# Optimization experiments

Measured on AMD Instinct MI355X. Metric: run time of the kernel, lower is better.

## Reference

```python
import jax, jax.numpy as jnp
import numpy as np

N_SRC, N_TGT, E, L, C_OUT = 100000, 200000, 500000, 256, 2


def setup_inputs() -> dict:
    key = jax.random.key(0)
    ks = jax.random.split(key, 10)
    s = 1.0 / np.sqrt(L)
    return {
        "pos_source": jax.random.normal(ks[0], (N_SRC, 3), jnp.float32),
        "pos_target": jax.random.normal(ks[1], (N_TGT, 3), jnp.float32),
        "latents": jax.random.normal(ks[2], (N_SRC, L), jnp.float32),
        "row": jax.random.randint(ks[3], (E,), 0, N_TGT),
        "col": jax.random.randint(ks[4], (E,), 0, N_SRC),
        "W_in": jax.random.normal(ks[5], (L + 3, L), jnp.float32) * s,
        "b_in": jnp.zeros((L,), jnp.float32),
        "W1": jax.random.normal(ks[6], (L, L), jnp.float32) * s,
        "b1": jnp.zeros((L,), jnp.float32),
        "W2": jax.random.normal(ks[7], (L, L), jnp.float32) * s,
        "b2": jnp.zeros((L,), jnp.float32),
        "W_out": jax.random.normal(ks[8], (L, C_OUT), jnp.float32) * s,
        "b_out": jnp.zeros((C_OUT,), jnp.float32),
    }


def reference(pos_source, pos_target, latents, row, col,
              W_in, b_in, W1, b1, W2, b2, W_out, b_out):
    # gather relative positions and latents per neighbor pair: [E, 3], [E, L]
    pos_rel = pos_target[row] - pos_source[col]
    x = jnp.concatenate([latents[col], pos_rel], axis=1)  # [E, L+3]
    x = x @ W_in + b_in                                   # fc_in
    x = jax.nn.relu(x) @ W1 + b1                          # mlp layer 0 (act first)
    x = jax.nn.relu(x) @ W2 + b2                          # mlp layer 1
    x = x @ W_out + b_out                                 # fc_out (no activation)
    return x[:, 0]                                        # predictions
```

## Files before the change

### kernel.cpp

```cpp
#include <hip/hip_runtime.h>
#include <hip/hip_bf16.h>
#include <stdint.h>

typedef __attribute__((ext_vector_type(8))) short bf16x8;
typedef __attribute__((ext_vector_type(4))) float f32x4;

#define NSRC 100000
#define WIN_OFF 0
#define W1P_OFF (128*1024)
#define BU_OFF  (256*1024)
#define SS_OFF  (BU_OFF + 2048)
#define Y_OFF   (264*1024)

#define PAIRB 1040
#define XBYTES (32*PAIRB)
#define POFF(r) (((r)>>1)*PAIRB + ((r)&1)*512)

#define L32 1040

#define AS3U32(p) ((__attribute__((address_space(3))) uint32_t*)(uintptr_t)(p))
#define AS1U32(p) ((const __attribute__((address_space(1))) uint32_t*)(uintptr_t)(p))

__global__ __launch_bounds__(256) void pack_kernel(
    const float* __restrict__ Win, const float* __restrict__ W1,
    const float* __restrict__ W2, const float* __restrict__ Wout,
    const float* __restrict__ b1, const float* __restrict__ b2,
    const float* __restrict__ b_out, char* __restrict__ wp)
{
    const int t = threadIdx.x, blk = blockIdx.x;
    if (blk < 16) {
        const float* W = (blk < 8) ? Win : W1;
        char* dst = wp + ((blk < 8) ? WIN_OFF : W1P_OFF);
        const int c = blk & 7;
        #pragma unroll
        for (int q = 0; q < 4; ++q) {
            union { bf16x8 v; __hip_bfloat16 h[8]; } u;
            #pragma unroll
            for (int j = 0; j < 8; ++j)
                u.h[j] = __float2bfloat16(W[(size_t)(c*32 + q*8 + j)*256 + t]);
            *(bf16x8*)(dst + c*16384 + t*64 + q*16) = u.v;
        }
    } else if (blk < 24) {
        __shared__ float w0s[256];
        w0s[t] = Wout[t*2];
        __syncthreads();
        const int b = blk - 16, fl = t >> 3, sub = t & 7, f = b*32 + fl;
        const float* row = W2 + (size_t)f*256 + sub*32;
        float p = 0.f;
        #pragma unroll
        for (int j = 0; j < 32; ++j) p += row[j]*w0s[sub*32 + j];
        p += __shfl_xor(p,1); p += __shfl_xor(p,2); p += __shfl_xor(p,4);
        if (sub == 0) {
            float2 v; v.x = b1[f]; v.y = p;
            *(float2*)(wp + BU_OFF + f*8) = v;
        }
    } else {
        __shared__ float rb[4];
        float v = b2[t]*Wout[t*2];
        v += __shfl_xor(v,1); v += __shfl_xor(v,2); v += __shfl_xor(v,4);
        v += __shfl_xor(v,8); v += __shfl_xor(v,16); v += __shfl_xor(v,32);
        if ((t&63) == 0) rb[t>>6] = v;
        __syncthreads();
        if (t == 0) *(float*)(wp + SS_OFF) = rb[0]+rb[1]+rb[2]+rb[3] + b_out[0];
    }
}

__global__ __launch_bounds__(256, 2) void precompute_y(
    const float* __restrict__ latents, const float* __restrict__ b_in,
    const char* __restrict__ wp, char* __restrict__ Yc)
{
    __shared__ __align__(16) char Ls[2][32*L32];
    __shared__ float binS[256];
    const int tid = threadIdx.x, wave = tid >> 6, lane = tid & 63;
    const int q = lane >> 4, lm = lane & 15;

    bf16x8 wA[4][8];
    {
        const char* wb = wp + WIN_OFF;
        #pragma unroll
        for (int mt = 0; mt < 4; ++mt) {
            const int m = wave*64 + mt*16 + lm;
            #pragma unroll
            for (int c = 0; c < 8; ++c)
                wA[mt][c] = *(const bf16x8*)(wb + c*16384 + m*64 + q*16);
        }
    }
    binS[tid] = b_in[tid];

    const int nt32 = NSRC / 32;
    const int t0 = blockIdx.x;

    #define STAGE32(t, buf) do {                                               \
        const float* __lat = latents + (size_t)(t)*32*256;                     \
        _Pragma("unroll")                                                      \
        for (int j = 0; j < 8; ++j) {                                          \
            const int r = wave*8 + j;                                          \
            __builtin_amdgcn_global_load_lds(                                  \
                AS1U32((const char*)(__lat + (size_t)r*256) + lane*16),        \
                AS3U32((buf) + r*L32), 16, 0, 0);                              \
        }                                                                      \
    } while (0)

    if (t0 < nt32) STAGE32(t0, Ls[0]);

    int it = 0;
    for (int t = t0; t < nt32; t += 512, ++it) {
        const int p = it & 1;
        __syncthreads();
        if (t + 512 < nt32) STAGE32(t + 512, Ls[1 - p]);

        f32x4 acc[4][2];
        #pragma unroll
        for (int mt = 0; mt < 4; ++mt)
            #pragma unroll
            for (int nt = 0; nt < 2; ++nt) acc[mt][nt] = (f32x4){0.f,0.f,0.f,0.f};

        const char* lb = Ls[p];
        #pragma unroll
        for (int c = 0; c < 8; ++c) {
            bf16x8 b[2];
            #pragma unroll
            for (int nt = 0; nt < 2; ++nt) {
                const int n = nt*16 + lm;
                const float* fp = (const float*)(lb + n*L32 + c*128 + q*32);
                float4 f0 = *(const float4*)fp;
                float4 f1 = *(const float4*)(fp + 4);
                union { bf16x8 v; __hip_bfloat16 h[8]; } u;
                u.h[0]=__float2bfloat16(f0.x); u.h[1]=__float2bfloat16(f0.y);
                u.h[2]=__float2bfloat16(f0.z); u.h[3]=__float2bfloat16(f0.w);
                u.h[4]=__float2bfloat16(f1.x); u.h[5]=__float2bfloat16(f1.y);
                u.h[6]=__float2bfloat16(f1.z); u.h[7]=__float2bfloat16(f1.w);
                b[nt] = u.v;
            }
            #pragma unroll
            for (int mt = 0; mt < 4; ++mt)
                #pragma unroll
                for (int nt = 0; nt < 2; ++nt)
                    acc[mt][nt] = __builtin_amdgcn_mfma_f32_16x16x32_bf16(wA[mt][c], b[nt], acc[mt][nt], 0,0,0);
        }
        #pragma unroll
        for (int mt = 0; mt < 4; ++mt) {
            const int f0 = wave*64 + mt*16 + q*4;
            float4 bb = *(const float4*)&binS[f0];
            float bbv[4] = {bb.x, bb.y, bb.z, bb.w};
            #pragma unroll
            for (int nt = 0; nt < 2; ++nt) {
                const int srow = t*32 + nt*16 + lm;
                union { uint2 uu; __hip_bfloat16 hh[4]; } pk;
                #pragma unroll
                for (int rg = 0; rg < 4; ++rg)
                    pk.hh[rg] = __float2bfloat16(acc[mt][nt][rg] + bbv[rg]);
                *(uint2*)(Yc + (size_t)srow*512 + f0*2) = pk.uu;
            }
        }
    }
    #undef STAGE32
}

__global__ __launch_bounds__(256, 2) void interp_main(
    const float* __restrict__ pos_src, const float* __restrict__ pos_tgt,
    const int* __restrict__ rowi, const int* __restrict__ coli,
    const float* __restrict__ Win, const char* __restrict__ wp,
    const char* __restrict__ Yc, float* __restrict__ out,
    int E, int ntiles)
{
    __shared__ __align__(16) char Xs[2][XBYTES];
    __shared__ float wposI[32][24];
    __shared__ float buS[512];
    __shared__ float posrel[2][64][4];
    __shared__ int   colsS[2][64];
    __shared__ float red[4][64];

    const int tid = threadIdx.x, wave = tid >> 6, lane = tid & 63;
    const int q = lane >> 4, lm = lane & 15;
    const int bid = blockIdx.x;

    bf16x8 wA[4][8];
    {
        const char* wb = wp + W1P_OFF;
        #pragma unroll
        for (int mt = 0; mt < 4; ++mt) {
            const int m = wave*64 + mt*16 + lm;
            #pragma unroll
            for (int c = 0; c < 8; ++c)
                wA[mt][c] = *(const bf16x8*)(wb + c*16384 + m*64 + q*16);
        }
    }
    {
        #pragma unroll
        for (int s = 0; s < 3; ++s)
            wposI[tid >> 3][s*8 + (tid & 7)] = Win[(size_t)(256+s)*256 + tid];
        *(float2*)&buS[tid*2] = *(const float2*)(wp + BU_OFF + tid*8);
    }
    const float Sv = *(const float*)(wp + SS_OFF);
    const int niter = (ntiles - bid + 511) / 512;

    #pragma unroll
    for (int ii = 0; ii < 2; ++ii) {
        if (tid < 64) {
            long tt = (long)bid + (long)ii*512; if (tt >= ntiles) tt = ntiles - 1;
            long e = tt*64 + tid; if (e >= E) e = E - 1;
            int ri = rowi[e], ci = coli[e];
            colsS[ii][tid] = ci;
            float4 pr;
            pr.x = pos_tgt[ri*3+0] - pos_src[ci*3+0];
            pr.y = pos_tgt[ri*3+1] - pos_src[ci*3+1];
            pr.z = pos_tgt[ri*3+2] - pos_src[ci*3+2];
            pr.w = 0.f;
            *(float4*)&posrel[ii][tid][0] = pr;
        }
    }
    __syncthreads();
    {
        #pragma unroll
        for (int k2 = 0; k2 < 8; ++k2) {
            const int r0 = wave*16 + k2*2;
            const int row = r0 + (lane >> 5);
            const int cv = colsS[0][row];
            const char* src = Yc + (size_t)cv*512 + (lane & 31)*16;
            __builtin_amdgcn_global_load_lds(AS1U32(src), AS3U32(Xs[0] + (r0>>1)*PAIRB), 16, 0, 0);
        }
    }

    for (int i = 0; i < niter; ++i) {
        const int p = i & 1;
        __syncthreads();

        if (i > 0 && tid < 64) {
            long e = ((long)bid + (long)(i-1)*512)*64 + tid;
            if (e < E) out[e] = red[0][tid]+red[1][tid]+red[2][tid]+red[3][tid] + Sv;
        }
        int m_ci = 0; float4 m_pr = {0.f,0.f,0.f,0.f};
        if (tid < 64) {
            long tt = (long)bid + (long)(i+2)*512; if (tt >= ntiles) tt = ntiles - 1;
            long e = tt*64 + tid; if (e >= E) e = E - 1;
            int ri = rowi[e]; m_ci = coli[e];
            m_pr.x = pos_tgt[ri*3+0] - pos_src[m_ci*3+0];
            m_pr.y = pos_tgt[ri*3+1] - pos_src[m_ci*3+1];
            m_pr.z = pos_tgt[ri*3+2] - pos_src[m_ci*3+2];
        }
        {
            const int fs = tid & 31, rb = tid >> 5;
            float w0v[8], w1v[8], w2v[8];
            {
                const float* wi = &wposI[fs][0];
                #pragma unroll
                for (int j = 0; j < 8; ++j) { w0v[j]=wi[j]; w1v[j]=wi[8+j]; w2v[j]=wi[16+j]; }
            }
            char* xb = Xs[p];
            #pragma unroll
            for (int ii2 = 0; ii2 < 8; ++ii2) {
                const int r = rb*8 + ii2;
                float4 pr = *(const float4*)&posrel[p][r][0];
                char* addr = xb + POFF(r) + fs*16;
                union { bf16x8 v; __hip_bfloat16 h[8]; } u;
                u.v = *(bf16x8*)addr;
                #pragma unroll
                for (int j = 0; j < 8; ++j) {
                    float vv = __bfloat162float(u.h[j]) + pr.x*w0v[j] + pr.y*w1v[j] + pr.z*w2v[j];
                    u.h[j] = __float2bfloat16(vv < 0.f ? 0.f : vv);
                }
                *(bf16x8*)addr = u.v;
            }
        }
        __syncthreads();

        {
            const int s = 1 - p;
            char* xb = Xs[s];
            #pragma unroll
            for (int k2 = 0; k2 < 8; ++k2) {
                const int r0 = wave*16 + k2*2;
                const int row = r0 + (lane >> 5);
                const int cv = colsS[s][row];
                const char* src = Yc + (size_t)cv*512 + (lane & 31)*16;
                __builtin_amdgcn_global_load_lds(AS1U32(src), AS3U32(xb + (r0>>1)*PAIRB), 16, 0, 0);
            }
        }
        f32x4 acc[4][4];
        #pragma unroll
        for (int mt = 0; mt < 4; ++mt)
            #pragma unroll
            for (int nt = 0; nt < 4; ++nt) acc[mt][nt] = (f32x4){0.f,0.f,0.f,0.f};
        {
            const char* xb = Xs[p];
            #pragma unroll
            for (int c = 0; c < 8; ++c) {
                bf16x8 b[4];
                #pragma unroll
                for (int nt = 0; nt < 4; ++nt)
                    b[nt] = *(const bf16x8*)(xb + POFF(nt*16+lm) + c*64 + q*16);
                #pragma unroll
                for (int mt = 0; mt < 4; ++mt)
                    #pragma unroll
                    for (int nt = 0; nt < 4; ++nt)
                        acc[mt][nt] = __builtin_amdgcn_mfma_f32_16x16x32_bf16(wA[mt][c], b[nt], acc[mt][nt], 0,0,0);
            }
        }
        float partial[4] = {0.f,0.f,0.f,0.f};
        #pragma unroll
        for (int mt = 0; mt < 4; ++mt) {
            const int f0 = wave*64 + mt*16 + q*4;
            float4 bu0 = *(const float4*)&buS[f0*2];
            float4 bu1 = *(const float4*)&buS[f0*2 + 4];
            float b1v[4] = {bu0.x, bu0.z, bu1.x, bu1.z};
            float uv[4]  = {bu0.y, bu0.w, bu1.y, bu1.w};
            #pragma unroll
            for (int nt = 0; nt < 4; ++nt)
                #pragma unroll
                for (int rg = 0; rg < 4; ++rg) {
                    float h = acc[mt][nt][rg] + b1v[rg];
                    if (h > 0.f) partial[nt] += h * uv[rg];
                }
        }
        #pragma unroll
        for (int nt = 0; nt < 4; ++nt) {
            float v = partial[nt];
            v += __shfl_xor(v, 16);
            v += __shfl_xor(v, 32);
            if (lane < 16) red[wave][nt*16 + lane] = v;
        }
        if (tid < 64) {
            colsS[p][tid] = m_ci;
            *(float4*)&posrel[p][tid][0] = m_pr;
        }
    }
    __syncthreads();
    if (tid < 64) {
        long e = ((long)bid + (long)(niter-1)*512)*64 + tid;
        if (e < E) out[e] = red[0][tid]+red[1][tid]+red[2][tid]+red[3][tid] + Sv;
    }
}

extern "C" void kernel_launch(void* const* d_in, const int* in_sizes, int n_in,
                              void* d_out, int out_size, void* d_ws, size_t ws_size,
                              hipStream_t stream)
{
    const float* pos_src = (const float*)d_in[0];
    const float* pos_tgt = (const float*)d_in[1];
    const float* latents = (const float*)d_in[2];
    const int*   rowi    = (const int*)d_in[3];
    const int*   coli    = (const int*)d_in[4];
    const float* Win     = (const float*)d_in[5];
    const float* b_in    = (const float*)d_in[6];
    const float* W1      = (const float*)d_in[7];
    const float* b1      = (const float*)d_in[8];
    const float* W2      = (const float*)d_in[9];
    const float* b2      = (const float*)d_in[10];
    const float* Wout    = (const float*)d_in[11];
    const float* b_out   = (const float*)d_in[12];
    float* out = (float*)d_out;
    const int E = in_sizes[3];
    const int ntiles = (E + 63) / 64;

    char* wp = (char*)d_ws;
    char* Yc = wp + Y_OFF;

    pack_kernel<<<25, 256, 0, stream>>>(Win, W1, W2, Wout, b1, b2, b_out, wp);
    precompute_y<<<512, 256, 0, stream>>>(latents, b_in, wp, Yc);
    interp_main<<<512, 256, 0, stream>>>(pos_src, pos_tgt, rowi, coli,
                                         Win, wp, Yc, out, E, ntiles);
}
```

Measured before the change: 304.5 us.

## Bucket edges by source-column group and stage group latents into LDS

Adds a slot kernel that bins edges into groups of 64 source columns using atomic counters, with a fixed per-group capacity. A new interp_col kernel stages each group's precomputed Y rows into LDS with one contiguous load, then processes that group's edges in tiles of 64. This replaces random per-edge 512-byte gathers of Y with coalesced loads. The cost is an extra atomic binning pass and padding waste in partially filled tiles. Any edges beyond the per-group capacity of 512 would be silently dropped.

Measured after the change: 448.0 us. +47.1%, slower.

```diff
diff --git a/kernel.cpp b/kernel.cpp
--- a/kernel.cpp
+++ b/kernel.cpp
@@ -12,6 +12,11 @@
 #define SS_OFF  (BU_OFF + 2048)
 #define Y_OFF   (264*1024)
 
+#define NG   1563
+#define CAP  512
+#define CNT_OFF  (Y_OFF + (size_t)NSRC*512 + 32768)
+#define SLOT_OFF (CNT_OFF + 8192)
+
 #define PAIRB 1040
 #define XBYTES (32*PAIRB)
 #define POFF(r) (((r)>>1)*PAIRB + ((r)&1)*512)
@@ -25,7 +30,8 @@
     const float* __restrict__ Win, const float* __restrict__ W1,
     const float* __restrict__ W2, const float* __restrict__ Wout,
     const float* __restrict__ b1, const float* __restrict__ b2,
-    const float* __restrict__ b_out, char* __restrict__ wp)
+    const float* __restrict__ b_out, char* __restrict__ wp,
+    int* __restrict__ cntA)
 {
     const int t = threadIdx.x, blk = blockIdx.x;
     if (blk < 16) {
@@ -54,7 +60,7 @@
             float2 v; v.x = b1[f]; v.y = p;
             *(float2*)(wp + BU_OFF + f*8) = v;
         }
-    } else {
+    } else if (blk == 24) {
         __shared__ float rb[4];
         float v = b2[t]*Wout[t*2];
         v += __shfl_xor(v,1); v += __shfl_xor(v,2); v += __shfl_xor(v,4);
@@ -62,6 +68,22 @@
         if ((t&63) == 0) rb[t>>6] = v;
         __syncthreads();
         if (t == 0) *(float*)(wp + SS_OFF) = rb[0]+rb[1]+rb[2]+rb[3] + b_out[0];
+    } else {
+        const int idx = (blk - 25)*256 + t;
+        if (idx < NG) cntA[idx] = 0;
+    }
+}
+
+__global__ __launch_bounds__(256) void slot_kernel(
+    const int* __restrict__ coli, int* __restrict__ cntA,
+    int* __restrict__ slots, int E)
+{
+    int i = blockIdx.x*256 + threadIdx.x;
+    for (; i < E; i += gridDim.x*256) {
+        const int c = coli[i];
+        const int g = c >> 6;
+        const int p = atomicAdd(&cntA[g], 1);
+        if (p < CAP) slots[(size_t)g*CAP + p] = (i << 6) | (c & 63);
     }
 }
 
@@ -155,6 +177,182 @@
         }
     }
     #undef STAGE32
+}
+
+__global__ __launch_bounds__(256, 2) void interp_col(
+    const float* __restrict__ pos_src, const float* __restrict__ pos_tgt,
+    const int* __restrict__ rowi, const float* __restrict__ Win,
+    const char* __restrict__ wp, const char* __restrict__ Yc,
+    const int* __restrict__ cntA, const int* __restrict__ slots,
+    float* __restrict__ out)
+{
+    __shared__ __align__(16) char Xs[XBYTES];
+    __shared__ __align__(16) char yS[64*512];
+    __shared__ float wposI[32][24];
+    __shared__ float buS[512];
+    __shared__ float posrel[64][4];
+    __shared__ int   lcS[64];
+    __shared__ float red[4][64];
+
+    const int tid = threadIdx.x, wave = tid >> 6, lane = tid & 63;
+    const int q = lane >> 4, lm = lane & 15;
+    const int bid = blockIdx.x;
+
+    bf16x8 wA[4][8];
+    {
+        const char* wb = wp + W1P_OFF;
+        #pragma unroll
+        for (int mt = 0; mt < 4; ++mt) {
+            const int m = wave*64 + mt*16 + lm;
+            #pragma unroll
+            for (int c = 0; c < 8; ++c)
+                wA[mt][c] = *(const bf16x8*)(wb + c*16384 + m*64 + q*16);
+        }
+    }
+    {
+        #pragma unroll
+        for (int s = 0; s < 3; ++s)
+            wposI[tid >> 3][s*8 + (tid & 7)] = Win[(size_t)(256+s)*256 + tid];
+        *(float2*)&buS[tid*2] = *(const float2*)(wp + BU_OFF + tid*8);
+    }
+    const float Sv = *(const float*)(wp + SS_OFF);
+
+    #define STAGE_Y(g) do {                                                    \
+        const char* __src = Yc + (size_t)(g)*32768;                            \
+        _Pragma("unroll")                                                      \
+        for (int j = 0; j < 8; ++j) {                                          \
+            const int base = j*4096 + wave*1024;                               \
+            __builtin_amdgcn_global_load_lds(                                  \
+                AS1U32(__src + base + lane*16), AS3U32(yS + base), 16, 0, 0);  \
+        }                                                                      \
+    } while (0)
+
+    #define CLAMPC(x) ((x) < 0 ? 0 : ((x) > CAP ? CAP : (x)))
+
+    #define META_LOAD(gm, tm, cm) do {                                         \
+        m_eid = -1; m_lc = 0;                                                  \
+        m_pr.x = 0.f; m_pr.y = 0.f; m_pr.z = 0.f; m_pr.w = 0.f;                \
+        if (tid < 64 && (gm) < NG) {                                           \
+            const int j = (tm)*64 + tid;                                       \
+            if (j < (cm)) {                                                    \
+                const int sv = slots[(size_t)(gm)*CAP + j];                    \
+                const int eid = sv >> 6;                                       \
+                m_lc = sv & 63;                                                \
+                const int ri = rowi[eid];                                      \
+                const int cc = (gm)*64 + m_lc;                                 \
+                m_pr.x = pos_tgt[ri*3+0] - pos_src[cc*3+0];                    \
+                m_pr.y = pos_tgt[ri*3+1] - pos_src[cc*3+1];                    \
+                m_pr.z = pos_tgt[ri*3+2] - pos_src[cc*3+2];                    \
+                m_eid = eid;                                                   \
+            }                                                                  \
+        }                                                                      \
+    } while (0)
+
+    int m_eid, m_lc; float4 m_pr;
+    int eidP = -1;
+
+    {
+        const int cg = CLAMPC(cntA[bid]);
+        STAGE_Y(bid);
+        META_LOAD(bid, 0, cg);
+    }
+
+    for (int g = bid; g < NG; g += 512) {
+        const int cnt0 = CLAMPC(cntA[g]);
+        int ntg = (cnt0 + 63) >> 6; if (ntg < 1) ntg = 1;
+        for (int t = 0; t < ntg; ++t) {
+            __syncthreads();
+            if (tid < 64) {
+                if (eidP >= 0)
+                    out[eidP] = red[0][tid]+red[1][tid]+red[2][tid]+red[3][tid] + Sv;
+                *(float4*)&posrel[tid][0] = m_pr;
+                lcS[tid] = m_lc;
+                eidP = m_eid;
+            }
+            __syncthreads();
+            {
+                const int fs = tid & 31, rb = tid >> 5;
+                float w0v[8], w1v[8], w2v[8];
+                {
+                    const float* wi = &wposI[fs][0];
+                    #pragma unroll
+                    for (int j = 0; j < 8; ++j) { w0v[j]=wi[j]; w1v[j]=wi[8+j]; w2v[j]=wi[16+j]; }
+                }
+                #pragma unroll
+                for (int ii2 = 0; ii2 < 8; ++ii2) {
+                    const int r = rb*8 + ii2;
+                    float4 pr = *(const float4*)&posrel[r][0];
+                    const int lc = lcS[r];
+                    union { bf16x8 v; __hip_bfloat16 h[8]; } u;
+                    u.v = *(const bf16x8*)(yS + lc*512 + fs*16);
+                    #pragma unroll
+                    for (int j = 0; j < 8; ++j) {
+                        float vv = __bfloat162float(u.h[j]) + pr.x*w0v[j] + pr.y*w1v[j] + pr.z*w2v[j];
+                        u.h[j] = __float2bfloat16(vv < 0.f ? 0.f : vv);
+                    }
+                    *(bf16x8*)(Xs + POFF(r) + fs*16) = u.v;
+                }
+            }
+            {
+                int gm, tm, cm;
+                if (t + 1 < ntg) { gm = g; tm = t + 1; cm = cnt0; }
+                else {
+                    gm = g + 512; tm = 0;
+                    cm = (gm < NG) ? CLAMPC(cntA[gm]) : 0;
+                }
+                META_LOAD(gm, tm, cm);
+            }
+            __syncthreads();
+            if (t == ntg - 1 && g + 512 < NG) STAGE_Y(g + 512);
+
+            f32x4 acc[4][4];
+            #pragma unroll
+            for (int mt = 0; mt < 4; ++mt)
+                #pragma unroll
+                for (int nt = 0; nt < 4; ++nt) acc[mt][nt] = (f32x4){0.f,0.f,0.f,0.f};
+            #pragma unroll
+            for (int c = 0; c < 8; ++c) {
+                bf16x8 b[4];
+                #pragma unroll
+                for (int nt = 0; nt < 4; ++nt)
+                    b[nt] = *(const bf16x8*)(Xs + POFF(nt*16+lm) + c*64 + q*16);
+                #pragma unroll
+                for (int mt = 0; mt < 4; ++mt)
+                    #pragma unroll
+                    for (int nt = 0; nt < 4; ++nt)
+                        acc[mt][nt] = __builtin_amdgcn_mfma_f32_16x16x32_bf16(wA[mt][c], b[nt], acc[mt][nt], 0,0,0);
+            }
+            float partial[4] = {0.f,0.f,0.f,0.f};
+            #pragma unroll
+            for (int mt = 0; mt < 4; ++mt) {
+                const int f0 = wave*64 + mt*16 + q*4;
+                float4 bu0 = *(const float4*)&buS[f0*2];
+                float4 bu1 = *(const float4*)&buS[f0*2 + 4];
+                float b1v[4] = {bu0.x, bu0.z, bu1.x, bu1.z};
+                float uv[4]  = {bu0.y, bu0.w, bu1.y, bu1.w};
+                #pragma unroll
+                for (int nt = 0; nt < 4; ++nt)
+                    #pragma unroll
+                    for (int rg = 0; rg < 4; ++rg) {
+                        float h = acc[mt][nt][rg] + b1v[rg];
+                        if (h > 0.f) partial[nt] += h * uv[rg];
+                    }
+            }
+            #pragma unroll
+            for (int nt = 0; nt < 4; ++nt) {
+                float v = partial[nt];
+                v += __shfl_xor(v, 16);
+                v += __shfl_xor(v, 32);
+                if (lane < 16) red[wave][nt*16 + lane] = v;
+            }
+        }
+    }
+    __syncthreads();
+    if (tid < 64 && eidP >= 0)
+        out[eidP] = red[0][tid]+red[1][tid]+red[2][tid]+red[3][tid] + Sv;
+    #undef STAGE_Y
+    #undef META_LOAD
+    #undef CLAMPC
 }
 
 __global__ __launch_bounds__(256, 2) void interp_main(
@@ -355,9 +553,21 @@
 
     char* wp = (char*)d_ws;
     char* Yc = wp + Y_OFF;
-
-    pack_kernel<<<25, 256, 0, stream>>>(Win, W1, W2, Wout, b1, b2, b_out, wp);
+    int* cntA  = (int*)(wp + CNT_OFF);
+    int* slots = (int*)(wp + SLOT_OFF);
+
+    const size_t need = SLOT_OFF + (size_t)NG*CAP*4;
+    const bool col_path = (ws_size >= need);
+
+    pack_kernel<<<col_path ? 33 : 25, 256, 0, stream>>>(
+        Win, W1, W2, Wout, b1, b2, b_out, wp, cntA);
+    if (col_path)
+        slot_kernel<<<512, 256, 0, stream>>>(coli, cntA, slots, E);
     precompute_y<<<512, 256, 0, stream>>>(latents, b_in, wp, Yc);
-    interp_main<<<512, 256, 0, stream>>>(pos_src, pos_tgt, rowi, coli,
-                                         Win, wp, Yc, out, E, ntiles);
+    if (col_path)
+        interp_col<<<512, 256, 0, stream>>>(pos_src, pos_tgt, rowi, Win, wp, Yc,
+                                            cntA, slots, out);
+    else
+        interp_main<<<512, 256, 0, stream>>>(pos_src, pos_tgt, rowi, coli,
+                                             Win, wp, Yc, out, E, ntiles);
 }
```

## Drop LDS double buffering and raise grid sizes for more resident blocks

Applied to the files above, without the earlier changes.

Both the precompute and main kernels switch from double-buffered LDS staging to a single buffer, loading each tile, syncing, then computing. This halves LDS use per block so more blocks can be resident, and the grids grow to 1024 and 768 blocks to fill that extra occupancy. Latency is meant to be hidden by having more blocks per CU rather than by prefetching inside a block. The cost is an extra barrier per iteration and no overlap of gather with MFMA within a block.

Result: slower. 329.3 us (+8.1%).

```diff
diff --git a/kernel.cpp b/kernel.cpp
--- a/kernel.cpp
+++ b/kernel.cpp
@@ -17,6 +17,9 @@
 #define POFF(r) (((r)>>1)*PAIRB + ((r)&1)*512)
 
 #define L32 1040
+
+#define IGRID 768
+#define PGRID 1024
 
 #define AS3U32(p) ((__attribute__((address_space(3))) uint32_t*)(uintptr_t)(p))
 #define AS1U32(p) ((const __attribute__((address_space(1))) uint32_t*)(uintptr_t)(p))
@@ -69,7 +72,7 @@
     const float* __restrict__ latents, const float* __restrict__ b_in,
     const char* __restrict__ wp, char* __restrict__ Yc)
 {
-    __shared__ __align__(16) char Ls[2][32*L32];
+    __shared__ __align__(16) char Ls[32*L32];
     __shared__ float binS[256];
     const int tid = threadIdx.x, wave = tid >> 6, lane = tid & 63;
     const int q = lane >> 4, lm = lane & 15;
@@ -88,26 +91,20 @@
     binS[tid] = b_in[tid];
 
     const int nt32 = NSRC / 32;
-    const int t0 = blockIdx.x;
-
-    #define STAGE32(t, buf) do {                                               \
-        const float* __lat = latents + (size_t)(t)*32*256;                     \
-        _Pragma("unroll")                                                      \
-        for (int j = 0; j < 8; ++j) {                                          \
-            const int r = wave*8 + j;                                          \
-            __builtin_amdgcn_global_load_lds(                                  \
-                AS1U32((const char*)(__lat + (size_t)r*256) + lane*16),        \
-                AS3U32((buf) + r*L32), 16, 0, 0);                              \
-        }                                                                      \
-    } while (0)
-
-    if (t0 < nt32) STAGE32(t0, Ls[0]);
-
-    int it = 0;
-    for (int t = t0; t < nt32; t += 512, ++it) {
-        const int p = it & 1;
-        __syncthreads();
-        if (t + 512 < nt32) STAGE32(t + 512, Ls[1 - p]);
+
+    for (int t = blockIdx.x; t < nt32; t += PGRID) {
+        __syncthreads();
+        {
+            const float* lat = latents + (size_t)t*32*256;
+            #pragma unroll
+            for (int j = 0; j < 8; ++j) {
+                const int r = wave*8 + j;
+                __builtin_amdgcn_global_load_lds(
+                    AS1U32((const char*)(lat + (size_t)r*256) + lane*16),
+                    AS3U32(Ls + r*L32), 16, 0, 0);
+            }
+        }
+        __syncthreads();
 
         f32x4 acc[4][2];
         #pragma unroll
@@ -115,14 +112,13 @@
             #pragma unroll
             for (int nt = 0; nt < 2; ++nt) acc[mt][nt] = (f32x4){0.f,0.f,0.f,0.f};
 
-        const char* lb = Ls[p];
         #pragma unroll
         for (int c = 0; c < 8; ++c) {
             bf16x8 b[2];
             #pragma unroll
             for (int nt = 0; nt < 2; ++nt) {
                 const int n = nt*16 + lm;
-                const float* fp = (const float*)(lb + n*L32 + c*128 + q*32);
+                const float* fp = (const float*)(Ls + n*L32 + c*128 + q*32);
                 float4 f0 = *(const float4*)fp;
                 float4 f1 = *(const float4*)(fp + 4);
                 union { bf16x8 v; __hip_bfloat16 h[8]; } u;
@@ -154,7 +150,6 @@
             }
         }
     }
-    #undef STAGE32
 }
 
 __global__ __launch_bounds__(256, 2) void interp_main(
@@ -164,7 +159,7 @@
     const char* __restrict__ Yc, float* __restrict__ out,
     int E, int ntiles)
 {
-    __shared__ __align__(16) char Xs[2][XBYTES];
+    __shared__ __align__(16) char Xs[XBYTES];
     __shared__ float wposI[32][24];
     __shared__ float buS[512];
     __shared__ float posrel[2][64][4];
@@ -193,12 +188,12 @@
         *(float2*)&buS[tid*2] = *(const float2*)(wp + BU_OFF + tid*8);
     }
     const float Sv = *(const float*)(wp + SS_OFF);
-    const int niter = (ntiles - bid + 511) / 512;
+    const int niter = (ntiles - bid + IGRID - 1) / IGRID;
 
     #pragma unroll
     for (int ii = 0; ii < 2; ++ii) {
         if (tid < 64) {
-            long tt = (long)bid + (long)ii*512; if (tt >= ntiles) tt = ntiles - 1;
+            long tt = (long)bid + (long)ii*IGRID; if (tt >= ntiles) tt = ntiles - 1;
             long e = tt*64 + tid; if (e >= E) e = E - 1;
             int ri = rowi[e], ci = coli[e];
             colsS[ii][tid] = ci;
@@ -210,29 +205,30 @@
             *(float4*)&posrel[ii][tid][0] = pr;
         }
     }
-    __syncthreads();
-    {
-        #pragma unroll
-        for (int k2 = 0; k2 < 8; ++k2) {
-            const int r0 = wave*16 + k2*2;
-            const int row = r0 + (lane >> 5);
-            const int cv = colsS[0][row];
-            const char* src = Yc + (size_t)cv*512 + (lane & 31)*16;
-            __builtin_amdgcn_global_load_lds(AS1U32(src), AS3U32(Xs[0] + (r0>>1)*PAIRB), 16, 0, 0);
-        }
-    }
 
     for (int i = 0; i < niter; ++i) {
         const int p = i & 1;
         __syncthreads();
 
+        {
+            #pragma unroll
+            for (int k2 = 0; k2 < 8; ++k2) {
+                const int r0 = wave*16 + k2*2;
+                const int row = r0 + (lane >> 5);
+                const int cv = colsS[p][row];
+                const char* src = Yc + (size_t)cv*512 + (lane & 31)*16;
+                __builtin_amdgcn_global_load_lds(AS1U32(src), AS3U32(Xs + (r0>>1)*PAIRB), 16, 0, 0);
+            }
+        }
+        __syncthreads();
+
         if (i > 0 && tid < 64) {
-            long e = ((long)bid + (long)(i-1)*512)*64 + tid;
+            long e = ((long)bid + (long)(i-1)*IGRID)*64 + tid;
             if (e < E) out[e] = red[0][tid]+red[1][tid]+red[2][tid]+red[3][tid] + Sv;
         }
         int m_ci = 0; float4 m_pr = {0.f,0.f,0.f,0.f};
         if (tid < 64) {
-            long tt = (long)bid + (long)(i+2)*512; if (tt >= ntiles) tt = ntiles - 1;
+            long tt = (long)bid + (long)(i+2)*IGRID; if (tt >= ntiles) tt = ntiles - 1;
             long e = tt*64 + tid; if (e >= E) e = E - 1;
             int ri = rowi[e]; m_ci = coli[e];
             m_pr.x = pos_tgt[ri*3+0] - pos_src[m_ci*3+0];
@@ -247,12 +243,11 @@
                 #pragma unroll
                 for (int j = 0; j < 8; ++j) { w0v[j]=wi[j]; w1v[j]=wi[8+j]; w2v[j]=wi[16+j]; }
             }
-            char* xb = Xs[p];
             #pragma unroll
             for (int ii2 = 0; ii2 < 8; ++ii2) {
                 const int r = rb*8 + ii2;
                 float4 pr = *(const float4*)&posrel[p][r][0];
-                char* addr = xb + POFF(r) + fs*16;
+                char* addr = Xs + POFF(r) + fs*16;
                 union { bf16x8 v; __hip_bfloat16 h[8]; } u;
                 u.v = *(bf16x8*)addr;
                 #pragma unroll
@@ -265,37 +260,22 @@
         }
         __syncthreads();
 
-        {
-            const int s = 1 - p;
-            char* xb = Xs[s];
-            #pragma unroll
-            for (int k2 = 0; k2 < 8; ++k2) {
-                const int r0 = wave*16 + k2*2;
-                const int row = r0 + (lane >> 5);
-                const int cv = colsS[s][row];
-                const char* src = Yc + (size_t)cv*512 + (lane & 31)*16;
-                __builtin_amdgcn_global_load_lds(AS1U32(src), AS3U32(xb + (r0>>1)*PAIRB), 16, 0, 0);
-            }
-        }
         f32x4 acc[4][4];
         #pragma unroll
         for (int mt = 0; mt < 4; ++mt)
             #pragma unroll
             for (int nt = 0; nt < 4; ++nt) acc[mt][nt] = (f32x4){0.f,0.f,0.f,0.f};
-        {
-            const char* xb = Xs[p];
-            #pragma unroll
-            for (int c = 0; c < 8; ++c) {
-                bf16x8 b[4];
+        #pragma unroll
+        for (int c = 0; c < 8; ++c) {
+            bf16x8 b[4];
+            #pragma unroll
+            for (int nt = 0; nt < 4; ++nt)
+                b[nt] = *(const bf16x8*)(Xs + POFF(nt*16+lm) + c*64 + q*16);
+            #pragma unroll
+            for (int mt = 0; mt < 4; ++mt)
                 #pragma unroll
                 for (int nt = 0; nt < 4; ++nt)
-                    b[nt] = *(const bf16x8*)(xb + POFF(nt*16+lm) + c*64 + q*16);
-                #pragma unroll
-                for (int mt = 0; mt < 4; ++mt)
-                    #pragma unroll
-                    for (int nt = 0; nt < 4; ++nt)
-                        acc[mt][nt] = __builtin_amdgcn_mfma_f32_16x16x32_bf16(wA[mt][c], b[nt], acc[mt][nt], 0,0,0);
-            }
+                    acc[mt][nt] = __builtin_amdgcn_mfma_f32_16x16x32_bf16(wA[mt][c], b[nt], acc[mt][nt], 0,0,0);
         }
         float partial[4] = {0.f,0.f,0.f,0.f};
         #pragma unroll
@@ -327,7 +307,7 @@
     }
     __syncthreads();
     if (tid < 64) {
-        long e = ((long)bid + (long)(niter-1)*512)*64 + tid;
+        long e = ((long)bid + (long)(niter-1)*IGRID)*64 + tid;
         if (e < E) out[e] = red[0][tid]+red[1][tid]+red[2][tid]+red[3][tid] + Sv;
     }
 }
@@ -357,7 +337,7 @@
     char* Yc = wp + Y_OFF;
 
     pack_kernel<<<25, 256, 0, stream>>>(Win, W1, W2, Wout, b1, b2, b_out, wp);
-    precompute_y<<<512, 256, 0, stream>>>(latents, b_in, wp, Yc);
-    interp_main<<<512, 256, 0, stream>>>(pos_src, pos_tgt, rowi, coli,
-                                         Win, wp, Yc, out, E, ntiles);
+    precompute_y<<<PGRID, 256, 0, stream>>>(latents, b_in, wp, Yc);
+    interp_main<<<IGRID, 256, 0, stream>>>(pos_src, pos_tgt, rowi, coli,
+                                           Win, wp, Yc, out, E, ntiles);
 }
```
